# Optimization experiments

Hardware: AMD Instinct MI355X
Metric: run time of the kernel (lower is better)

Reference implementation:

```python
import jax, jax.numpy as jnp
import numpy as np

B, N, CHANNELS = 4, 2048, 512
HEADS, HEAD_DIM = 8, 64
HIDDEN = HEADS * HEAD_DIM
ROPE_THETA = 10000.0


def _rotate_half(x):
    # interleaved pairs, as in rotary_embedding_torch
    x1 = x[..., 0::2]
    x2 = x[..., 1::2]
    return jnp.stack((-x2, x1), axis=-1).reshape(x.shape)


def _rope(x):
    # x: [b, h, n, d]; rotate over seq axis -2, full head dim
    n, d = x.shape[-2], x.shape[-1]
    inv_freq = 1.0 / (ROPE_THETA ** (jnp.arange(0, d, 2, dtype=jnp.float32) / d))
    freqs = jnp.arange(n, dtype=jnp.float32)[:, None] * inv_freq  # [n, d/2]
    freqs = jnp.repeat(freqs, 2, axis=-1)  # [n, d]
    return x * jnp.cos(freqs) + _rotate_half(x) * jnp.sin(freqs)


def setup_inputs() -> dict:
    key = jax.random.key(0)
    k1, k2, k3, k4 = jax.random.split(key, 4)
    x = jax.random.normal(k1, (B, N, CHANNELS), dtype=jnp.float32)
    pos_bias = jax.random.normal(k2, (HEADS, N, N), dtype=jnp.float32) * 0.02
    w_qkv = jax.random.normal(k3, (3 * HIDDEN, CHANNELS), dtype=jnp.float32) / np.sqrt(CHANNELS)
    w_out = jax.random.normal(k4, (CHANNELS, HIDDEN), dtype=jnp.float32) / np.sqrt(HIDDEN)
    return {"x": x, "pos_bias": pos_bias, "w_qkv": w_qkv, "w_out": w_out}


def reference(x, pos_bias, w_qkv, w_out):
    scale = HEAD_DIM ** -0.5
    b, n, _ = x.shape
    qkv = x @ w_qkv.T  # [b, n, 3*hidden]
    q, k, v = jnp.split(qkv, 3, axis=-1)

    def split_heads(z):
        return z.reshape(b, n, HEADS, HEAD_DIM).transpose(0, 2, 1, 3)  # [b,h,n,d]

    q, k, v = map(split_heads, (q, k, v))
    q = q * scale
    q = _rope(q)
    k = _rope(k)
    sim = jnp.einsum('bhid,bhjd->bhij', q, k) + pos_bias  # pos_bias [h,n,n] broadcasts
    attn = jax.nn.softmax(sim, axis=-1)  # matches sim - amax(detached) then softmax
    out = jnp.einsum('bhij,bhjd->bhid', attn, v)
    out = out.transpose(0, 2, 1, 3).reshape(b, n, HIDDEN)
    return out @ w_out.T
```

## Files before the change

### kernel.cpp

```cpp
#include <hip/hip_runtime.h>
#include <hip/hip_bf16.h>
#include <math.h>

typedef __bf16 bf16;
typedef bf16  bf16x8 __attribute__((ext_vector_type(8)));
typedef bf16  bf16x4 __attribute__((ext_vector_type(4)));
typedef float f32x4  __attribute__((ext_vector_type(4)));
typedef float f32x16 __attribute__((ext_vector_type(16)));

#define B_   4
#define N_   2048
#define CH_  512
#define H_   8
#define D_   64
#define HID_ 512

__device__ __forceinline__ f32x4 mfma16(bf16x8 a, bf16x8 b, f32x4 c) {
    return __builtin_amdgcn_mfma_f32_16x16x32_bf16(a, b, c, 0, 0, 0);
}
__device__ __forceinline__ f32x16 mfma32(bf16x8 a, bf16x8 b, f32x16 c) {
    return __builtin_amdgcn_mfma_f32_32x32x16_bf16(a, b, c, 0, 0, 0);
}

__global__ void rope_table_k(float* __restrict__ cosT, float* __restrict__ sinT) {
    int idx = blockIdx.x * 256 + threadIdx.x;
    int pos = idx >> 5, fi = idx & 31;
    double inv = pow(10000.0, -(double)(2 * fi) / 64.0);
    double ang = (double)pos * inv;
    cosT[idx] = (float)cos(ang);
    sinT[idx] = (float)sin(ang);
}

__global__ __launch_bounds__(256) void qkv_rope_k(
    const float* __restrict__ x, const float* __restrict__ w,
    const float* __restrict__ cosT, const float* __restrict__ sinT,
    bf16* __restrict__ Qb, bf16* __restrict__ Kb, bf16* __restrict__ Vt)
{
    __shared__ __align__(16) bf16 Xs[128][40];
    __shared__ __align__(16) bf16 Ws[128][40];
    const int tid = threadIdx.x, lane = tid & 63, wid = tid >> 6;
    const int wr = wid >> 1, wc = wid & 1;
    const int m0 = blockIdx.x * 128, n0 = blockIdx.y * 128;
    const int l15 = lane & 15, l4 = lane >> 4;
    const int sr = tid >> 1, sh = (tid & 1) * 16;

    f32x4 acc[4][4] = {};

    for (int kt = 0; kt < 16; ++kt) {
        __syncthreads();
        {
            const float4* xp = reinterpret_cast<const float4*>(x + (size_t)(m0 + sr) * CH_ + kt * 32 + sh);
            const float4* wp = reinterpret_cast<const float4*>(w + (size_t)(n0 + sr) * CH_ + kt * 32 + sh);
#pragma unroll
            for (int j = 0; j < 4; ++j) {
                float4 f = xp[j];
                bf16x4 o1 = { (bf16)f.x, (bf16)f.y, (bf16)f.z, (bf16)f.w };
                *reinterpret_cast<bf16x4*>(&Xs[sr][sh + j * 4]) = o1;
                float4 g = wp[j];
                bf16x4 o2 = { (bf16)g.x, (bf16)g.y, (bf16)g.z, (bf16)g.w };
                *reinterpret_cast<bf16x4*>(&Ws[sr][sh + j * 4]) = o2;
            }
        }
        __syncthreads();
        bf16x8 a[4], bb[4];
#pragma unroll
        for (int mf = 0; mf < 4; ++mf)
            a[mf] = *reinterpret_cast<const bf16x8*>(&Xs[wr * 64 + mf * 16 + l15][l4 * 8]);
#pragma unroll
        for (int nf = 0; nf < 4; ++nf)
            bb[nf] = *reinterpret_cast<const bf16x8*>(&Ws[wc * 64 + nf * 16 + l15][l4 * 8]);
#pragma unroll
        for (int mf = 0; mf < 4; ++mf)
#pragma unroll
            for (int nf = 0; nf < 4; ++nf)
                acc[mf][nf] = mfma16(a[mf], bb[nf], acc[mf][nf]);
    }

#pragma unroll
    for (int nf = 0; nf < 4; ++nf) {
        const int col = n0 + wc * 64 + nf * 16 + l15;
        const int sec = col >> 9;
        const int cc = col & 511;
        const int hh = cc >> 6, dd = cc & 63;
        if (sec == 2) {
#pragma unroll
            for (int mf = 0; mf < 4; ++mf) {
                const int pos0 = m0 + wr * 64 + mf * 16 + l4 * 4;
                const int bb_ = pos0 >> 11, pos = pos0 & 2047;
                bf16x4 pk = { (bf16)acc[mf][nf][0], (bf16)acc[mf][nf][1],
                              (bf16)acc[mf][nf][2], (bf16)acc[mf][nf][3] };
                *reinterpret_cast<bf16x4*>(
                    Vt + ((size_t)(bb_ * H_ + hh) * D_ + dd) * N_ + pos) = pk;
            }
        } else {
            const float sgn = (dd & 1) ? 1.f : -1.f;
#pragma unroll
            for (int mf = 0; mf < 4; ++mf) {
#pragma unroll
                for (int i = 0; i < 4; ++i) {
                    const int row = m0 + wr * 64 + mf * 16 + l4 * 4 + i;
                    const int bb_ = row >> 11, pos = row & 2047;
                    const float v = acc[mf][nf][i];
                    const float v2 = __shfl_xor(v, 1);
                    const size_t dst = ((size_t)((bb_ * H_ + hh) * N_ + pos)) * D_ + dd;
                    const float c = cosT[pos * 32 + (dd >> 1)];
                    const float s = sinT[pos * 32 + (dd >> 1)];
                    const float r = v * c + sgn * v2 * s;
                    if (sec == 0) Qb[dst] = (bf16)(r * 0.125f);
                    else          Kb[dst] = (bf16)r;
                }
            }
        }
    }
}

#define KRD2(kt2,kc) (((kt2)*32 + l31)*128 + (((kc)*32 + l5*16) ^ (l7<<4)))
#define VRD2(dt,kt)  (((dt)*32 + l31)*128 + (((kt)*32 + l5*16) ^ (l7<<4)))
#define PRD2(kt)     (wid*4096 + l31*128 + (((kt)*32 + l5*16) ^ (l7<<4)))
#define PST2(kt2,r2) (wid*4096 + l31*128 + (((kt2)*64 + (r2)*16 + l5*8) ^ (l7<<4)))

__global__ __launch_bounds__(256, 4) void attn_k(
    const bf16* __restrict__ Qb, const bf16* __restrict__ Kb, const bf16* __restrict__ Vt,
    const float* __restrict__ bias, bf16* __restrict__ AO)
{
    __shared__ __align__(16) unsigned char KsB[2][8192];
    __shared__ __align__(16) unsigned char VsB[2][8192];
    __shared__ __align__(16) unsigned char PwB[4][4096];

    const int tid = threadIdx.x, lane = tid & 63, wid = tid >> 6;
    const int l31 = lane & 31, l5 = lane >> 5, l7 = lane & 7;
    const int id = blockIdx.x;
    const int xcd = id & 7, j = id >> 3;
    const int bh = xcd + 8 * (j >> 4);
    const int qt = j & 15;
    const int b = bh >> 3, h = bh & 7;
    const int q0 = qt * 128 + wid * 32;
    const size_t bhoff = (size_t)bh * N_ * D_;

    bf16x8 qreg[4];
#pragma unroll
    for (int kc = 0; kc < 4; ++kc)
        qreg[kc] = *reinterpret_cast<const bf16x8*>(
            Qb + bhoff + (size_t)(q0 + l31) * D_ + kc * 16 + l5 * 8);

    const unsigned scol = ((lane & 7) * 16) ^ ((lane >> 3) << 4);
    const char* kg = (const char*)(Kb + bhoff) + (size_t)(wid * 8 + (lane >> 3)) * 128 + scol;
    const char* vg = (const char*)(Vt + bhoff) + (size_t)(wid * 8 + (lane >> 3)) * (N_ * 2) + scol;

    const float* bp = bias + ((size_t)h * N_ + (q0 + l31)) * N_ + l5 * 4;

    unsigned char* pwD = &PwB[0][0];

#define GLL(src, dst) __builtin_amdgcn_global_load_lds( \
        (const __attribute__((address_space(1))) unsigned int*)(src), \
        (__attribute__((address_space(3))) unsigned int*)(dst), 16, 0, 0)

#define STAGE(buf, t) do { \
        GLL(kg + (size_t)(t) * 8192,          &KsB[buf][wid * 1024]); \
        GLL(kg + (size_t)(t) * 8192 + 4096,   &KsB[buf][4096 + wid * 1024]); \
        GLL(vg + (size_t)(t) * 128,           &VsB[buf][wid * 1024]); \
        GLL(vg + (size_t)(t) * 128 + 131072,  &VsB[buf][4096 + wid * 1024]); \
    } while (0)

    f32x16 o[2] = {};
    float lp = 0.f;
    f32x4 bc[2][4], bn[2][4];

    STAGE(0, 0);
#pragma unroll
    for (int kt2 = 0; kt2 < 2; ++kt2)
#pragma unroll
        for (int r2 = 0; r2 < 4; ++r2)
            bc[kt2][r2] = *reinterpret_cast<const f32x4*>(bp + kt2 * 32 + r2 * 8);
    __syncthreads();

#pragma unroll 2
    for (int kb = 0; kb < 32; ++kb) {
        const int cur = kb & 1;
        if (kb < 31) {
            STAGE(cur ^ 1, kb + 1);
#pragma unroll
            for (int kt2 = 0; kt2 < 2; ++kt2)
#pragma unroll
                for (int r2 = 0; r2 < 4; ++r2)
                    bn[kt2][r2] = *reinterpret_cast<const f32x4*>(
                        bp + (size_t)(kb + 1) * 64 + kt2 * 32 + r2 * 8);
        }

        const unsigned char* ksC = &KsB[cur][0];
        f32x16 s[2] = {};
        __builtin_amdgcn_s_setprio(1);
#pragma unroll
        for (int kt2 = 0; kt2 < 2; ++kt2) {
#pragma unroll
            for (int kc = 0; kc < 4; ++kc) {
                bf16x8 kf = *reinterpret_cast<const bf16x8*>(ksC + KRD2(kt2, kc));
                s[kt2] = mfma32(kf, qreg[kc], s[kt2]);
            }
        }
        __builtin_amdgcn_s_setprio(0);

#pragma unroll
        for (int kt2 = 0; kt2 < 2; ++kt2) {
#pragma unroll
            for (int r2 = 0; r2 < 4; ++r2) {
                float p0 = __expf(s[kt2][r2 * 4 + 0] + bc[kt2][r2][0]);
                float p1 = __expf(s[kt2][r2 * 4 + 1] + bc[kt2][r2][1]);
                float p2 = __expf(s[kt2][r2 * 4 + 2] + bc[kt2][r2][2]);
                float p3 = __expf(s[kt2][r2 * 4 + 3] + bc[kt2][r2][3]);
                lp += (p0 + p1) + (p2 + p3);
                bf16x4 pk = { (bf16)p0, (bf16)p1, (bf16)p2, (bf16)p3 };
                *reinterpret_cast<bf16x4*>(pwD + PST2(kt2, r2)) = pk;
            }
        }

        const unsigned char* vsC = &VsB[cur][0];
        __builtin_amdgcn_s_setprio(1);
#pragma unroll
        for (int kt = 0; kt < 4; ++kt) {
            bf16x8 pa = *reinterpret_cast<const bf16x8*>(pwD + PRD2(kt));
#pragma unroll
            for (int dt = 0; dt < 2; ++dt) {
                bf16x8 vf = *reinterpret_cast<const bf16x8*>(vsC + VRD2(dt, kt));
                o[dt] = mfma32(pa, vf, o[dt]);
            }
        }
        __builtin_amdgcn_s_setprio(0);

#pragma unroll
        for (int kt2 = 0; kt2 < 2; ++kt2)
#pragma unroll
            for (int r2 = 0; r2 < 4; ++r2)
                bc[kt2][r2] = bn[kt2][r2];
        __syncthreads();
    }

    float tot = lp;
    tot += __shfl_xor(tot, 32);
    float rv[16];
#pragma unroll
    for (int reg = 0; reg < 16; ++reg) {
        const int qr = (reg & 3) + 8 * (reg >> 2) + 4 * l5;
        rv[reg] = 1.0f / __shfl(tot, qr);
    }
#pragma unroll
    for (int dt = 0; dt < 2; ++dt)
#pragma unroll
        for (int reg = 0; reg < 16; ++reg) {
            const int qr = (reg & 3) + 8 * (reg >> 2) + 4 * l5;
            AO[((size_t)(b * N_ + q0 + qr)) * HID_ + h * D_ + dt * 32 + l31] =
                (bf16)(o[dt][reg] * rv[reg]);
        }
}

__global__ __launch_bounds__(256) void proj_k(
    const bf16* __restrict__ A, const float* __restrict__ w, float* __restrict__ out)
{
    __shared__ __align__(16) bf16 As[128][40];
    __shared__ __align__(16) bf16 Ws[128][40];
    const int tid = threadIdx.x, lane = tid & 63, wid = tid >> 6;
    const int wr = wid >> 1, wc = wid & 1;
    const int m0 = blockIdx.x * 128, n0 = blockIdx.y * 128;
    const int l15 = lane & 15, l4 = lane >> 4;
    const int sr = tid >> 1, sh = (tid & 1) * 16;

    f32x4 acc[4][4] = {};

    for (int kt = 0; kt < 16; ++kt) {
        __syncthreads();
        {
            const bf16* ap = A + (size_t)(m0 + sr) * HID_ + kt * 32 + sh;
            *reinterpret_cast<bf16x8*>(&As[sr][sh])     = *reinterpret_cast<const bf16x8*>(ap);
            *reinterpret_cast<bf16x8*>(&As[sr][sh + 8]) = *reinterpret_cast<const bf16x8*>(ap + 8);
            const float4* wp = reinterpret_cast<const float4*>(w + (size_t)(n0 + sr) * HID_ + kt * 32 + sh);
#pragma unroll
            for (int j = 0; j < 4; ++j) {
                float4 g = wp[j];
                bf16x4 o2 = { (bf16)g.x, (bf16)g.y, (bf16)g.z, (bf16)g.w };
                *reinterpret_cast<bf16x4*>(&Ws[sr][sh + j * 4]) = o2;
            }
        }
        __syncthreads();
        bf16x8 a[4], bb[4];
#pragma unroll
        for (int mf = 0; mf < 4; ++mf)
            a[mf] = *reinterpret_cast<const bf16x8*>(&As[wr * 64 + mf * 16 + l15][l4 * 8]);
#pragma unroll
        for (int nf = 0; nf < 4; ++nf)
            bb[nf] = *reinterpret_cast<const bf16x8*>(&Ws[wc * 64 + nf * 16 + l15][l4 * 8]);
#pragma unroll
        for (int mf = 0; mf < 4; ++mf)
#pragma unroll
            for (int nf = 0; nf < 4; ++nf)
                acc[mf][nf] = mfma16(a[mf], bb[nf], acc[mf][nf]);
    }
#pragma unroll
    for (int nf = 0; nf < 4; ++nf) {
        const int col = n0 + wc * 64 + nf * 16 + l15;
#pragma unroll
        for (int mf = 0; mf < 4; ++mf) {
#pragma unroll
            for (int i = 0; i < 4; ++i) {
                const int row = m0 + wr * 64 + mf * 16 + l4 * 4 + i;
                out[(size_t)row * HID_ + col] = acc[mf][nf][i];
            }
        }
    }
}

extern "C" void kernel_launch(void* const* d_in, const int* in_sizes, int n_in,
                              void* d_out, int out_size, void* d_ws, size_t ws_size,
                              hipStream_t stream) {
    (void)in_sizes; (void)n_in; (void)out_size; (void)ws_size;
    const float* x     = (const float*)d_in[0];
    const float* bias  = (const float*)d_in[1];
    const float* w_qkv = (const float*)d_in[2];
    const float* w_out = (const float*)d_in[3];
    float* out = (float*)d_out;

    bf16* Qb = (bf16*)d_ws;
    bf16* Kb = Qb + 4194304;
    bf16* Vt = Kb + 4194304;
    bf16* AO = Vt + 4194304;
    float* cosT = (float*)(AO + 4194304);
    float* sinT = cosT + 65536;

    rope_table_k<<<dim3(256), 256, 0, stream>>>(cosT, sinT);
    qkv_rope_k  <<<dim3(64, 12), 256, 0, stream>>>(x, w_qkv, cosT, sinT, Qb, Kb, Vt);
    attn_k      <<<dim3(512), 256, 0, stream>>>(Qb, Kb, Vt, bias, AO);
    proj_k      <<<dim3(64, 4), 256, 0, stream>>>(AO, w_out, out);
}
```

Baseline: 158.0 us.

## Split attention keys across two waves and read K/V directly from global memory

```diff
diff --git a/kernel.cpp b/kernel.cpp
--- a/kernel.cpp
+++ b/kernel.cpp
@@ -114,27 +114,26 @@
     }
 }
 
-#define KRD2(kt2,kc) (((kt2)*32 + l31)*128 + (((kc)*32 + l5*16) ^ (l7<<4)))
-#define VRD2(dt,kt)  (((dt)*32 + l31)*128 + (((kt)*32 + l5*16) ^ (l7<<4)))
-#define PRD2(kt)     (wid*4096 + l31*128 + (((kt)*32 + l5*16) ^ (l7<<4)))
-#define PST2(kt2,r2) (wid*4096 + l31*128 + (((kt2)*64 + (r2)*16 + l5*8) ^ (l7<<4)))
-
-__global__ __launch_bounds__(256, 4) void attn_k(
+#define PSTR(kt2,r2) (l31*128 + (((kt2)*64 + (r2)*16 + l5*8) ^ (l7<<4)))
+#define PRDR(kt)     (l31*128 + (((kt)*32 + l5*16) ^ (l7<<4)))
+
+__global__ __launch_bounds__(128, 4) void attn_k(
     const bf16* __restrict__ Qb, const bf16* __restrict__ Kb, const bf16* __restrict__ Vt,
     const float* __restrict__ bias, bf16* __restrict__ AO)
 {
-    __shared__ __align__(16) unsigned char KsB[2][8192];
-    __shared__ __align__(16) unsigned char VsB[2][8192];
-    __shared__ __align__(16) unsigned char PwB[4][4096];
+    __shared__ __align__(16) unsigned char PwB[2][4096];
+    __shared__ __align__(16) float Ored[32][64];
+    __shared__ float Lred[32];
 
     const int tid = threadIdx.x, lane = tid & 63, wid = tid >> 6;
     const int l31 = lane & 31, l5 = lane >> 5, l7 = lane & 7;
     const int id = blockIdx.x;
     const int xcd = id & 7, j = id >> 3;
-    const int bh = xcd + 8 * (j >> 4);
-    const int qt = j & 15;
+    const int bh = xcd + 8 * (j >> 6);
+    const int qt = j & 63;
     const int b = bh >> 3, h = bh & 7;
-    const int q0 = qt * 128 + wid * 32;
+    const int q0 = qt * 32;
+    const int k0 = wid * 1024;
     const size_t bhoff = (size_t)bh * N_ * D_;
 
     bf16x8 qreg[4];
@@ -143,58 +142,24 @@
         qreg[kc] = *reinterpret_cast<const bf16x8*>(
             Qb + bhoff + (size_t)(q0 + l31) * D_ + kc * 16 + l5 * 8);
 
-    const unsigned scol = ((lane & 7) * 16) ^ ((lane >> 3) << 4);
-    const char* kg = (const char*)(Kb + bhoff) + (size_t)(wid * 8 + (lane >> 3)) * 128 + scol;
-    const char* vg = (const char*)(Vt + bhoff) + (size_t)(wid * 8 + (lane >> 3)) * (N_ * 2) + scol;
-
-    const float* bp = bias + ((size_t)h * N_ + (q0 + l31)) * N_ + l5 * 4;
-
-    unsigned char* pwD = &PwB[0][0];
-
-#define GLL(src, dst) __builtin_amdgcn_global_load_lds( \
-        (const __attribute__((address_space(1))) unsigned int*)(src), \
-        (__attribute__((address_space(3))) unsigned int*)(dst), 16, 0, 0)
-
-#define STAGE(buf, t) do { \
-        GLL(kg + (size_t)(t) * 8192,          &KsB[buf][wid * 1024]); \
-        GLL(kg + (size_t)(t) * 8192 + 4096,   &KsB[buf][4096 + wid * 1024]); \
-        GLL(vg + (size_t)(t) * 128,           &VsB[buf][wid * 1024]); \
-        GLL(vg + (size_t)(t) * 128 + 131072,  &VsB[buf][4096 + wid * 1024]); \
-    } while (0)
+    const bf16* Kp = Kb + bhoff + (size_t)k0 * D_;
+    const bf16* Vp = Vt + bhoff + k0;
+    const float* bp = bias + ((size_t)h * N_ + q0 + l31) * N_ + k0 + l5 * 4;
+
+    unsigned char* pwD = &PwB[wid][0];
 
     f32x16 o[2] = {};
     float lp = 0.f;
-    f32x4 bc[2][4], bn[2][4];
-
-    STAGE(0, 0);
-#pragma unroll
-    for (int kt2 = 0; kt2 < 2; ++kt2)
-#pragma unroll
-        for (int r2 = 0; r2 < 4; ++r2)
-            bc[kt2][r2] = *reinterpret_cast<const f32x4*>(bp + kt2 * 32 + r2 * 8);
-    __syncthreads();
-
-#pragma unroll 2
-    for (int kb = 0; kb < 32; ++kb) {
-        const int cur = kb & 1;
-        if (kb < 31) {
-            STAGE(cur ^ 1, kb + 1);
-#pragma unroll
-            for (int kt2 = 0; kt2 < 2; ++kt2)
-#pragma unroll
-                for (int r2 = 0; r2 < 4; ++r2)
-                    bn[kt2][r2] = *reinterpret_cast<const f32x4*>(
-                        bp + (size_t)(kb + 1) * 64 + kt2 * 32 + r2 * 8);
-        }
-
-        const unsigned char* ksC = &KsB[cur][0];
+
+    for (int kb = 0; kb < 16; ++kb) {
         f32x16 s[2] = {};
         __builtin_amdgcn_s_setprio(1);
 #pragma unroll
         for (int kt2 = 0; kt2 < 2; ++kt2) {
 #pragma unroll
             for (int kc = 0; kc < 4; ++kc) {
-                bf16x8 kf = *reinterpret_cast<const bf16x8*>(ksC + KRD2(kt2, kc));
+                bf16x8 kf = *reinterpret_cast<const bf16x8*>(
+                    Kp + (size_t)(kb * 64 + kt2 * 32 + l31) * D_ + kc * 16 + l5 * 8);
                 s[kt2] = mfma32(kf, qreg[kc], s[kt2]);
             }
         }
@@ -204,53 +169,59 @@
         for (int kt2 = 0; kt2 < 2; ++kt2) {
 #pragma unroll
             for (int r2 = 0; r2 < 4; ++r2) {
-                float p0 = __expf(s[kt2][r2 * 4 + 0] + bc[kt2][r2][0]);
-                float p1 = __expf(s[kt2][r2 * 4 + 1] + bc[kt2][r2][1]);
-                float p2 = __expf(s[kt2][r2 * 4 + 2] + bc[kt2][r2][2]);
-                float p3 = __expf(s[kt2][r2 * 4 + 3] + bc[kt2][r2][3]);
+                f32x4 bc = *reinterpret_cast<const f32x4*>(bp + kb * 64 + kt2 * 32 + r2 * 8);
+                float p0 = __expf(s[kt2][r2 * 4 + 0] + bc[0]);
+                float p1 = __expf(s[kt2][r2 * 4 + 1] + bc[1]);
+                float p2 = __expf(s[kt2][r2 * 4 + 2] + bc[2]);
+                float p3 = __expf(s[kt2][r2 * 4 + 3] + bc[3]);
                 lp += (p0 + p1) + (p2 + p3);
                 bf16x4 pk = { (bf16)p0, (bf16)p1, (bf16)p2, (bf16)p3 };
-                *reinterpret_cast<bf16x4*>(pwD + PST2(kt2, r2)) = pk;
-            }
-        }
-
-        const unsigned char* vsC = &VsB[cur][0];
+                *reinterpret_cast<bf16x4*>(pwD + PSTR(kt2, r2)) = pk;
+            }
+        }
+
         __builtin_amdgcn_s_setprio(1);
 #pragma unroll
         for (int kt = 0; kt < 4; ++kt) {
-            bf16x8 pa = *reinterpret_cast<const bf16x8*>(pwD + PRD2(kt));
+            bf16x8 pa = *reinterpret_cast<const bf16x8*>(pwD + PRDR(kt));
 #pragma unroll
             for (int dt = 0; dt < 2; ++dt) {
-                bf16x8 vf = *reinterpret_cast<const bf16x8*>(vsC + VRD2(dt, kt));
+                bf16x8 vf = *reinterpret_cast<const bf16x8*>(
+                    Vp + (size_t)(dt * 32 + l31) * N_ + kb * 64 + kt * 16 + l5 * 8);
                 o[dt] = mfma32(pa, vf, o[dt]);
             }
         }
         __builtin_amdgcn_s_setprio(0);
-
-#pragma unroll
-        for (int kt2 = 0; kt2 < 2; ++kt2)
-#pragma unroll
-            for (int r2 = 0; r2 < 4; ++r2)
-                bc[kt2][r2] = bn[kt2][r2];
-        __syncthreads();
     }
 
     float tot = lp;
     tot += __shfl_xor(tot, 32);
-    float rv[16];
-#pragma unroll
-    for (int reg = 0; reg < 16; ++reg) {
-        const int qr = (reg & 3) + 8 * (reg >> 2) + 4 * l5;
-        rv[reg] = 1.0f / __shfl(tot, qr);
-    }
-#pragma unroll
-    for (int dt = 0; dt < 2; ++dt)
-#pragma unroll
-        for (int reg = 0; reg < 16; ++reg) {
-            const int qr = (reg & 3) + 8 * (reg >> 2) + 4 * l5;
-            AO[((size_t)(b * N_ + q0 + qr)) * HID_ + h * D_ + dt * 32 + l31] =
-                (bf16)(o[dt][reg] * rv[reg]);
-        }
+
+    if (wid == 1) {
+#pragma unroll
+        for (int dt = 0; dt < 2; ++dt)
+#pragma unroll
+            for (int reg = 0; reg < 16; ++reg) {
+                const int qr = (reg & 3) + 8 * (reg >> 2) + 4 * l5;
+                Ored[qr][dt * 32 + l31] = o[dt][reg];
+            }
+        if (lane < 32) Lred[lane] = tot;
+    }
+    __syncthreads();
+
+    if (wid == 0) {
+        const float dv = tot + Lred[l31];
+#pragma unroll
+        for (int dt = 0; dt < 2; ++dt)
+#pragma unroll
+            for (int reg = 0; reg < 16; ++reg) {
+                const int qr = (reg & 3) + 8 * (reg >> 2) + 4 * l5;
+                const float ov = o[dt][reg] + Ored[qr][dt * 32 + l31];
+                const float dn = __shfl(dv, qr);
+                AO[((size_t)(b * N_ + q0 + qr)) * HID_ + h * D_ + dt * 32 + l31] =
+                    (bf16)(ov / dn);
+            }
+    }
 }
 
 __global__ __launch_bounds__(256) void proj_k(
@@ -327,6 +298,6 @@
 
     rope_table_k<<<dim3(256), 256, 0, stream>>>(cosT, sinT);
     qkv_rope_k  <<<dim3(64, 12), 256, 0, stream>>>(x, w_qkv, cosT, sinT, Qb, Kb, Vt);
-    attn_k      <<<dim3(512), 256, 0, stream>>>(Qb, Kb, Vt, bias, AO);
+    attn_k      <<<dim3(2048), 128, 0, stream>>>(Qb, Kb, Vt, bias, AO);
     proj_k      <<<dim3(64, 4), 256, 0, stream>>>(AO, w_out, out);
 }
```

New measurement: 252.6 us. +59.8%, slower.
